# Kernel tuning notes

Hardware: AMD Instinct MI355X
Metric: run time of the kernel (lower is better)

Reference implementation:

```python
import jax, jax.numpy as jnp
import numpy as np

B, J, D, T = 4096, 22, 3, 50  # batch, joints, xyz dims, seq_len
N = J * D                     # 66 channels
LW = 3                        # local_window
TAU = 5.0
EPS = 1e-5


def _chain_adj_mask(n):
    m = np.zeros((n, n), dtype=np.float32)
    for i in range(n - 1):
        m[i, i + 1] = 1.0
        m[i + 1, i] = 1.0
    return m


def _band_mask(t, w):
    i = np.arange(t)
    return (np.abs(i[:, None] - i[None, :]) <= w).astype(np.float32)


def setup_inputs() -> dict:
    key = jax.random.key(0)
    ks = jax.random.split(key, 9)
    x = jax.random.normal(ks[0], (B, N, T), dtype=jnp.float32)
    adj = jnp.eye(J, dtype=jnp.float32) + 0.1 * jax.random.normal(ks[1], (J, J), dtype=jnp.float32)
    adj_t = 0.1 * jax.random.normal(ks[2], (T, T), dtype=jnp.float32)
    adj_jc = 0.1 * jax.random.normal(ks[3], (J, D, D), dtype=jnp.float32)
    adj_tj = 0.1 * jax.random.normal(ks[4], (N, T, T), dtype=jnp.float32)
    mlp = jax.random.normal(ks[5], (T, 4), dtype=jnp.float32)
    w_update = 1e-2 * jax.random.normal(ks[6], (T, T), dtype=jnp.float32)
    b_update = jnp.zeros((T,), dtype=jnp.float32)
    alpha = jnp.ones((1, N, 1), dtype=jnp.float32)
    beta = jnp.zeros((1, N, 1), dtype=jnp.float32)
    adj_mask = jnp.asarray(_chain_adj_mask(J))
    traj_mask = jnp.asarray(_band_mask(T, LW))
    u = jax.random.uniform(ks[7], (B, 4), minval=1e-6, maxval=1.0 - 1e-6, dtype=jnp.float32)
    gumbels = -jnp.log(-jnp.log(u))
    return {"x": x, "adj": adj, "adj_t": adj_t, "adj_jc": adj_jc, "adj_tj": adj_tj,
            "mlp": mlp, "w_update": w_update, "b_update": b_update,
            "alpha": alpha, "beta": beta, "adj_mask": adj_mask,
            "traj_mask": traj_mask, "gumbels": gumbels}


def reference(x, adj, adj_t, adj_jc, adj_tj, mlp, w_update, b_update,
              alpha, beta, adj_mask, traj_mask, gumbels):
    xr = x.reshape(B, J, D, T)
    # spatial GC: masked joint-joint adjacency
    x1 = jnp.einsum('vj,bjct->bvct', adj * adj_mask, xr).reshape(B, N, T)
    # temporal GC: banded time-time adjacency shared over channels
    x2 = jnp.einsum('ft,bnt->bnf', adj_t * traj_mask, x)
    # joint-channel GC: per-joint 3x3 channel mixing
    x3 = jnp.einsum('jkc,bjct->bjkt', adj_jc, xr).reshape(B, N, T)
    # spatio-temporal GC: per-channel banded time-time adjacency
    x4 = jnp.einsum('nft,bnt->bnf', adj_tj * traj_mask[None], x)
    # gate: mean-pool over channels -> [B,T] @ [T,4], hard gumbel-softmax
    prob = x.mean(axis=1) @ mlp
    y = jax.nn.softmax((prob + gumbels) / TAU, axis=-1)
    y_hard = jax.nn.one_hot(jnp.argmax(y, axis=-1), 4, dtype=y.dtype)
    gate = y_hard + y - jax.lax.stop_gradient(y)  # straight-through
    # option 0 is zeros, so only options 1..3 contribute
    x_ = (gate[:, 1, None, None] * x2
          + gate[:, 2, None, None] * x3
          + gate[:, 3, None, None] * x4)
    # update linear along time axis
    x_ = (x1 + x_) @ w_update.T + b_update
    # spatial LayerNorm over channel axis
    mean = x_.mean(axis=1, keepdims=True)
    var = ((x_ - mean) ** 2).mean(axis=1, keepdims=True)
    x_ = (x_ - mean) / jnp.sqrt(var + EPS) * alpha + beta
    return x + x_
```

## Files before the change

kernel.cpp:

```cpp
#include <hip/hip_runtime.h>


typedef __attribute__((ext_vector_type(8))) short short8_t;
typedef __attribute__((ext_vector_type(4))) float f32x4_t;

__device__ __forceinline__ unsigned short f2bf(float f) {
    unsigned u = __float_as_uint(f);
    u += 0x7fffu + ((u >> 16) & 1u);
    return (unsigned short)(u >> 16);
}
__device__ __forceinline__ float bf2f(unsigned us) {
    return __uint_as_float(us << 16);
}

#define XLD(nn, tt) (*(const uint2*)((const char*)xbf + (((((nn) << 6) + (tt)) << 1) ^ (((nn) & 7) << 4))))

__global__ __launch_bounds__(256) void pack_kernel(
    const float* __restrict__ adj_t,
    const float* __restrict__ adj_tj,
    unsigned short* __restrict__ ws)
{
    int i = blockIdx.x * 256 + threadIdx.x;
    if (i < 400) {
        int f = i >> 3, j = i & 7;
        int tt = f - 3 + j;
        float v = (j < 7 && tt >= 0 && tt < 50) ? adj_t[f * 50 + tt] : 0.f;
        ws[i] = f2bf(v);
    } else if (i < 26800) {
        int e = i - 400;
        int nf = e >> 3, j = e & 7;
        int f = nf % 50;
        int tt = f - 3 + j;
        float v = (j < 7 && tt >= 0 && tt < 50) ? adj_tj[(size_t)nf * 50 + tt] : 0.f;
        ws[i] = f2bf(v);
    }
}

__global__ __launch_bounds__(256, 2) void dyn_kernel(
    const float* __restrict__ x,
    const float* __restrict__ adj,
    const float* __restrict__ adj_t,
    const float* __restrict__ adj_jc,
    const float* __restrict__ adj_tj,
    const float* __restrict__ mlp,
    const float* __restrict__ w_update,
    const float* __restrict__ alpha,
    const float* __restrict__ beta,
    const float* __restrict__ gumbels,
    const unsigned short* __restrict__ wpack,
    int packed,
    float* __restrict__ out)
{
    __shared__ unsigned short xbf[66 * 64];
    __shared__ unsigned short zbf[66 * 64];
    __shared__ float wsum[16];
    __shared__ float as[66], bs[66];

    const int b    = blockIdx.x;
    const int tid  = threadIdx.x;
    const int lane = tid & 63;
    const int wv   = tid >> 6;
    const int li   = lane & 15;
    const int lq   = lane >> 4;
    const int f    = wv * 16 + li;
    const float* __restrict__ xb = x + (size_t)b * 3300;

    const float4 gv = *(const float4*)(gumbels + (size_t)b * 4);

    int sn[4], st0[4], sv[4];
    float cwm[4], cwp[4];
    #pragma unroll
    for (int r = 0; r < 4; ++r) {
        int i = tid + (r << 8);
        if (r == 3 && i > 857) i = 857;
        int n = i / 13, q = i - n * 13;
        sn[r] = n; st0[r] = q * 4;
        int v = n / 3; sv[r] = v;
        cwm[r] = (v > 0)  ? adj[v * 22 + v - 1] : 0.f;
        cwp[r] = (v < 21) ? adj[v * 22 + v + 1] : 0.f;
    }

    short8_t bfrag0, bfrag1;
    #pragma unroll
    for (int j = 0; j < 8; ++j) {
        int k0 = 8 * lq + j;
        int k1 = 32 + 8 * lq + j;
        float v0 = (f < 50) ? w_update[f * 50 + k0] : 0.f;
        float v1 = (f < 50 && k1 < 50) ? w_update[f * 50 + k1] : 0.f;
        bfrag0[j] = (short)f2bf(v0);
        bfrag1[j] = (short)f2bf(v1);
    }

    for (int i = tid; i < 198; i += 256) {
        int n = i / 3, p = i - n * 3;
        int t0 = 52 + p * 4;
        int byteoff = ((n * 64 + t0) * 2) ^ ((n & 7) << 4);
        uint2 z2; z2.x = 0u; z2.y = 0u;
        *(uint2*)((char*)xbf + byteoff) = z2;
        *(uint2*)((char*)zbf + byteoff) = z2;
    }
    if (tid < 66) { as[tid] = alpha[tid]; bs[tid] = beta[tid]; }

    float2 xa[4], xc[4];
    #pragma unroll
    for (int r = 0; r < 4; ++r) {
        int off = sn[r] * 50 + st0[r];
        xa[r] = *(const float2*)(xb + off);
        int off2 = off + 2; if (off2 > 3298) off2 = 3298;
        xc[r] = *(const float2*)(xb + off2);
    }
    float4 pl = {0.f, 0.f, 0.f, 0.f};
    const float4* __restrict__ mlp4 = (const float4*)mlp;
    #pragma unroll
    for (int r = 0; r < 4; ++r) {
        int n = sn[r], t0 = st0[r];
        bool full = (t0 < 48);
        float v0 = xa[r].x, v1 = xa[r].y;
        float v2 = full ? xc[r].x : 0.f;
        float v3 = full ? xc[r].y : 0.f;
        float4 m0 = mlp4[t0], m1 = mlp4[t0 + 1];
        int i2 = t0 + 2; if (i2 > 49) i2 = 49;
        int i3 = t0 + 3; if (i3 > 49) i3 = 49;
        float4 m2 = mlp4[i2], m3 = mlp4[i3];
        if (r < 3 || tid < 90) {
            pl.x += v0 * m0.x + v1 * m1.x + v2 * m2.x + v3 * m3.x;
            pl.y += v0 * m0.y + v1 * m1.y + v2 * m2.y + v3 * m3.y;
            pl.z += v0 * m0.z + v1 * m1.z + v2 * m2.z + v3 * m3.z;
            pl.w += v0 * m0.w + v1 * m1.w + v2 * m2.w + v3 * m3.w;
        }
        uint2 pk;
        pk.x = (unsigned)f2bf(v0) | ((unsigned)f2bf(v1) << 16);
        pk.y = (unsigned)f2bf(v2) | ((unsigned)f2bf(v3) << 16);
        *(uint2*)((char*)xbf + (((n * 64 + t0) * 2) ^ ((n & 7) << 4))) = pk;
    }
    #pragma unroll
    for (int d = 1; d < 64; d <<= 1) {
        pl.x += __shfl_xor(pl.x, d, 64);
        pl.y += __shfl_xor(pl.y, d, 64);
        pl.z += __shfl_xor(pl.z, d, 64);
        pl.w += __shfl_xor(pl.w, d, 64);
    }
    if (lane == 0) *(float4*)&wsum[wv * 4] = pl;
    __syncthreads();

    int g;
    {
        float4 s0 = *(const float4*)&wsum[0],  s1 = *(const float4*)&wsum[4];
        float4 s2 = *(const float4*)&wsum[8],  s3 = *(const float4*)&wsum[12];
        const float inv = 1.0f / 66.0f;
        float l0 = (s0.x + s1.x + s2.x + s3.x) * inv + gv.x;
        float l1 = (s0.y + s1.y + s2.y + s3.y) * inv + gv.y;
        float l2 = (s0.z + s1.z + s2.z + s3.z) * inv + gv.z;
        float l3 = (s0.w + s1.w + s2.w + s3.w) * inv + gv.w;
        g = 0; float bv = l0;
        if (l1 > bv) { bv = l1; g = 1; }
        if (l2 > bv) { bv = l2; g = 2; }
        if (l3 > bv) { bv = l3; g = 3; }
    }

    if (g == 1 || g == 3) {
        uint4 w0[4], w1[4];
        auto loadrows = [&](int r, uint4* dst) {
            if (packed) {
                const uint4* wt4 = (const uint4*)
                    ((g == 1) ? wpack : wpack + 400 + (size_t)sn[r] * 400);
                #pragma unroll
                for (int k = 0; k < 4; ++k) {
                    int ff = st0[r] + k; if (ff > 49) ff = 49;
                    dst[k] = wt4[ff];
                }
            } else {
                const float* rb = (g == 1) ? adj_t : (adj_tj + (size_t)sn[r] * 2500);
                #pragma unroll
                for (int k = 0; k < 4; ++k) {
                    int ff = st0[r] + k; if (ff > 49) ff = 49;
                    float w[8];
                    #pragma unroll
                    for (int j = 0; j < 8; ++j) {
                        int tt = ff - 3 + j;
                        w[j] = (j < 7 && tt >= 0 && tt < 50) ? rb[ff * 50 + tt] : 0.f;
                    }
                    uint4 u;
                    u.x = (unsigned)f2bf(w[0]) | ((unsigned)f2bf(w[1]) << 16);
                    u.y = (unsigned)f2bf(w[2]) | ((unsigned)f2bf(w[3]) << 16);
                    u.z = (unsigned)f2bf(w[4]) | ((unsigned)f2bf(w[5]) << 16);
                    u.w = (unsigned)f2bf(w[6]) | ((unsigned)f2bf(w[7]) << 16);
                    dst[k] = u;
                }
            }
        };
        loadrows(0, w0);
        #pragma unroll
        for (int r = 0; r < 4; ++r) {
            uint4* wcur = (r & 1) ? w1 : w0;
            uint4* wnxt = (r & 1) ? w0 : w1;
            if (r < 3) loadrows(r + 1, wnxt);
            int n = sn[r], t0 = st0[r];
            uint2 pm = {0u, 0u}, pp = {0u, 0u};
            if (n >= 3)  pm = XLD(n - 3, t0);
            if (n <= 62) pp = XLD(n + 3, t0);
            float acc0 = cwm[r] * bf2f(pm.x & 0xffff) + cwp[r] * bf2f(pp.x & 0xffff);
            float acc1 = cwm[r] * bf2f(pm.x >> 16)    + cwp[r] * bf2f(pp.x >> 16);
            float acc2 = cwm[r] * bf2f(pm.y & 0xffff) + cwp[r] * bf2f(pp.y & 0xffff);
            float acc3 = cwm[r] * bf2f(pm.y >> 16)    + cwp[r] * bf2f(pp.y >> 16);
            float xr[12];
            if (t0 >= 4) {
                uint2 p0 = XLD(n, t0 - 4);
                xr[0] = bf2f(p0.x & 0xffff); xr[1] = bf2f(p0.x >> 16);
                xr[2] = bf2f(p0.y & 0xffff); xr[3] = bf2f(p0.y >> 16);
            } else { xr[0] = 0.f; xr[1] = 0.f; xr[2] = 0.f; xr[3] = 0.f; }
            {
                uint2 p1 = XLD(n, t0);
                xr[4] = bf2f(p1.x & 0xffff); xr[5] = bf2f(p1.x >> 16);
                xr[6] = bf2f(p1.y & 0xffff); xr[7] = bf2f(p1.y >> 16);
            }
            {
                uint2 p2 = XLD(n, t0 + 4);
                xr[8]  = bf2f(p2.x & 0xffff); xr[9]  = bf2f(p2.x >> 16);
                xr[10] = bf2f(p2.y & 0xffff); xr[11] = bf2f(p2.y >> 16);
            }
            #pragma unroll
            for (int j = 0; j < 4; ++j) {
                int ff = t0 + j;
                if (ff < 50) {
                    uint4 u = wcur[j];
                    float a = bf2f(u.x & 0xffff) * xr[j + 1]
                            + bf2f(u.x >> 16)    * xr[j + 2]
                            + bf2f(u.y & 0xffff) * xr[j + 3]
                            + bf2f(u.y >> 16)    * xr[j + 4]
                            + bf2f(u.z & 0xffff) * xr[j + 5]
                            + bf2f(u.z >> 16)    * xr[j + 6]
                            + bf2f(u.w & 0xffff) * xr[j + 7];
                    if (j == 0) acc0 += a; else if (j == 1) acc1 += a;
                    else if (j == 2) acc2 += a; else acc3 += a;
                }
            }
            uint2 pk;
            pk.x = (unsigned)f2bf(acc0) | ((unsigned)f2bf(acc1) << 16);
            pk.y = (unsigned)f2bf(acc2) | ((unsigned)f2bf(acc3) << 16);
            *(uint2*)((char*)zbf + (((n * 64 + t0) * 2) ^ ((n & 7) << 4))) = pk;
        }
    } else {
        #pragma unroll
        for (int r = 0; r < 4; ++r) {
            int n = sn[r], t0 = st0[r], v = sv[r];
            uint2 pm = {0u, 0u}, pp = {0u, 0u};
            if (n >= 3)  pm = XLD(n - 3, t0);
            if (n <= 62) pp = XLD(n + 3, t0);
            float acc0 = cwm[r] * bf2f(pm.x & 0xffff) + cwp[r] * bf2f(pp.x & 0xffff);
            float acc1 = cwm[r] * bf2f(pm.x >> 16)    + cwp[r] * bf2f(pp.x >> 16);
            float acc2 = cwm[r] * bf2f(pm.y & 0xffff) + cwp[r] * bf2f(pp.y & 0xffff);
            float acc3 = cwm[r] * bf2f(pm.y >> 16)    + cwp[r] * bf2f(pp.y >> 16);
            if (g == 2) {
                int c = n - v * 3;
                const float* ajc = adj_jc + (size_t)(v * 3 + c) * 3;
                #pragma unroll
                for (int cc = 0; cc < 3; ++cc) {
                    float w = ajc[cc];
                    uint2 p = XLD(v * 3 + cc, t0);
                    acc0 += w * bf2f(p.x & 0xffff); acc1 += w * bf2f(p.x >> 16);
                    acc2 += w * bf2f(p.y & 0xffff); acc3 += w * bf2f(p.y >> 16);
                }
            }
            uint2 pk;
            pk.x = (unsigned)f2bf(acc0) | ((unsigned)f2bf(acc1) << 16);
            pk.y = (unsigned)f2bf(acc2) | ((unsigned)f2bf(acc3) << 16);
            *(uint2*)((char*)zbf + (((n * 64 + t0) * 2) ^ ((n & 7) << 4))) = pk;
        }
    }
    __syncthreads();

    f32x4_t dacc[5];
    #pragma unroll
    for (int mt = 0; mt < 5; ++mt) dacc[mt] = (f32x4_t){0.f, 0.f, 0.f, 0.f};

    #pragma unroll
    for (int ks = 0; ks < 2; ++ks) {
        short8_t bfrag = ks ? bfrag1 : bfrag0;
        #pragma unroll
        for (int mt = 0; mt < 5; ++mt) {
            int m = mt * 16 + li;
            short8_t afrag = {0, 0, 0, 0, 0, 0, 0, 0};
            if (m < 66)
                afrag = *(const short8_t*)((const char*)zbf + (((m * 64 + 8 * lq + 32 * ks) * 2) ^ ((m & 7) << 4)));
            dacc[mt] = __builtin_amdgcn_mfma_f32_16x16x32_bf16(afrag, bfrag, dacc[mt], 0, 0, 0);
        }
    }

    float S = 0.f, SS = 0.f;
    #pragma unroll
    for (int mt = 0; mt < 5; ++mt) {
        #pragma unroll
        for (int r = 0; r < 4; ++r) {
            int m = mt * 16 + lq * 4 + r;
            if (mt < 4 || m < 66) { float d = dacc[mt][r]; S += d; SS += d * d; }
        }
    }
    S  += __shfl_xor(S, 16, 64);  S  += __shfl_xor(S, 32, 64);
    SS += __shfl_xor(SS, 16, 64); SS += __shfl_xor(SS, 32, 64);
    const float mean = S * (1.f / 66.f);
    const float var  = SS * (1.f / 66.f) - mean * mean;
    const float rstd = rsqrtf(var + 1e-5f);

    if (f < 50) {
        float* __restrict__ ob = out + (size_t)b * 3300;
        #pragma unroll
        for (int mt = 0; mt < 5; ++mt) {
            #pragma unroll
            for (int r = 0; r < 4; ++r) {
                int m = mt * 16 + lq * 4 + r;
                if (mt < 4 || m < 66) {
                    unsigned short xu = *(const unsigned short*)
                        ((const char*)xbf + (((m * 64 + f) * 2) ^ ((m & 7) << 4)));
                    float xv = bf2f((unsigned)xu);
                    float xn = (dacc[mt][r] - mean) * rstd;
                    ob[m * 50 + f] = xv + xn * as[m] + bs[m];
                }
            }
        }
    }
}

extern "C" void kernel_launch(void* const* d_in, const int* in_sizes, int n_in,
                              void* d_out, int out_size, void* d_ws, size_t ws_size,
                              hipStream_t stream) {
    (void)in_sizes; (void)n_in; (void)out_size;
    const float* x        = (const float*)d_in[0];
    const float* adj      = (const float*)d_in[1];
    const float* adj_t    = (const float*)d_in[2];
    const float* adj_jc   = (const float*)d_in[3];
    const float* adj_tj   = (const float*)d_in[4];
    const float* mlp      = (const float*)d_in[5];
    const float* w_update = (const float*)d_in[6];
    const float* alpha    = (const float*)d_in[8];
    const float* beta     = (const float*)d_in[9];
    const float* gumbels  = (const float*)d_in[12];

    const size_t pack_bytes = (size_t)26800 * sizeof(unsigned short);
    int packed = (d_ws != nullptr && ws_size >= pack_bytes) ? 1 : 0;
    unsigned short* ws = (unsigned short*)d_ws;
    if (packed)
        pack_kernel<<<105, 256, 0, stream>>>(adj_t, adj_tj, ws);

    dyn_kernel<<<4096, 256, 0, stream>>>(x, adj, adj_t, adj_jc, adj_tj, mlp,
                                         w_update, alpha, beta, gumbels,
                                         ws, packed, (float*)d_out);
}
```

Measured before the change: 58.56 us.

## Process two batch samples per block to amortize setup and weight loads

Each block now handles two consecutive batch elements, with double-sized LDS buffers for the bf16 input and intermediate tiles. The per-block setup (index tables, w_update B-fragments, alpha/beta, LDS padding) is shared across both samples, and both samples' global loads are issued up front to raise memory-level parallelism. The grid is halved to 2048 blocks, which doubles LDS use per block and raises register pressure. That can lower occupancy and leave the tail less evenly spread across CUs.

New measurement: 66.04 us. 1.13x slower.

```diff
diff --git a/kernel.cpp b/kernel.cpp
--- a/kernel.cpp
+++ b/kernel.cpp
@@ -12,8 +12,9 @@
 __device__ __forceinline__ float bf2f(unsigned us) {
     return __uint_as_float(us << 16);
 }
-
-#define XLD(nn, tt) (*(const uint2*)((const char*)xbf + (((((nn) << 6) + (tt)) << 1) ^ (((nn) & 7) << 4))))
+__device__ __forceinline__ uint2 xld(const unsigned short* base, int n, int t) {
+    return *(const uint2*)((const char*)base + (((n * 64 + t) * 2) ^ ((n & 7) << 4)));
+}
 
 __global__ __launch_bounds__(256) void pack_kernel(
     const float* __restrict__ adj_t,
@@ -51,21 +52,23 @@
     int packed,
     float* __restrict__ out)
 {
-    __shared__ unsigned short xbf[66 * 64];
-    __shared__ unsigned short zbf[66 * 64];
-    __shared__ float wsum[16];
+    __shared__ unsigned short xls[2][66 * 64];
+    __shared__ unsigned short zls[2][66 * 64];
+    __shared__ float wsum[2][16];
     __shared__ float as[66], bs[66];
 
-    const int b    = blockIdx.x;
     const int tid  = threadIdx.x;
     const int lane = tid & 63;
     const int wv   = tid >> 6;
     const int li   = lane & 15;
     const int lq   = lane >> 4;
     const int f    = wv * 16 + li;
-    const float* __restrict__ xb = x + (size_t)b * 3300;
-
-    const float4 gv = *(const float4*)(gumbels + (size_t)b * 4);
+    const int b0   = blockIdx.x * 2;
+    const float* __restrict__ xb0 = x + (size_t)b0 * 3300;
+    const float* __restrict__ xb1 = xb0 + 3300;
+
+    const float4 gv0 = *(const float4*)(gumbels + (size_t)b0 * 4);
+    const float4 gv1 = *(const float4*)(gumbels + (size_t)b0 * 4 + 4);
 
     int sn[4], st0[4], sv[4];
     float cwm[4], cwp[4];
@@ -96,225 +99,246 @@
         int t0 = 52 + p * 4;
         int byteoff = ((n * 64 + t0) * 2) ^ ((n & 7) << 4);
         uint2 z2; z2.x = 0u; z2.y = 0u;
-        *(uint2*)((char*)xbf + byteoff) = z2;
-        *(uint2*)((char*)zbf + byteoff) = z2;
+        *(uint2*)((char*)xls[0] + byteoff) = z2;
+        *(uint2*)((char*)xls[1] + byteoff) = z2;
+        *(uint2*)((char*)zls[0] + byteoff) = z2;
+        *(uint2*)((char*)zls[1] + byteoff) = z2;
     }
     if (tid < 66) { as[tid] = alpha[tid]; bs[tid] = beta[tid]; }
 
-    float2 xa[4], xc[4];
+    float2 xa[2][4], xc[2][4];
     #pragma unroll
     for (int r = 0; r < 4; ++r) {
         int off = sn[r] * 50 + st0[r];
-        xa[r] = *(const float2*)(xb + off);
         int off2 = off + 2; if (off2 > 3298) off2 = 3298;
-        xc[r] = *(const float2*)(xb + off2);
-    }
-    float4 pl = {0.f, 0.f, 0.f, 0.f};
+        xa[0][r] = *(const float2*)(xb0 + off);
+        xc[0][r] = *(const float2*)(xb0 + off2);
+        xa[1][r] = *(const float2*)(xb1 + off);
+        xc[1][r] = *(const float2*)(xb1 + off2);
+    }
     const float4* __restrict__ mlp4 = (const float4*)mlp;
     #pragma unroll
-    for (int r = 0; r < 4; ++r) {
-        int n = sn[r], t0 = st0[r];
-        bool full = (t0 < 48);
-        float v0 = xa[r].x, v1 = xa[r].y;
-        float v2 = full ? xc[r].x : 0.f;
-        float v3 = full ? xc[r].y : 0.f;
-        float4 m0 = mlp4[t0], m1 = mlp4[t0 + 1];
-        int i2 = t0 + 2; if (i2 > 49) i2 = 49;
-        int i3 = t0 + 3; if (i3 > 49) i3 = 49;
-        float4 m2 = mlp4[i2], m3 = mlp4[i3];
-        if (r < 3 || tid < 90) {
-            pl.x += v0 * m0.x + v1 * m1.x + v2 * m2.x + v3 * m3.x;
-            pl.y += v0 * m0.y + v1 * m1.y + v2 * m2.y + v3 * m3.y;
-            pl.z += v0 * m0.z + v1 * m1.z + v2 * m2.z + v3 * m3.z;
-            pl.w += v0 * m0.w + v1 * m1.w + v2 * m2.w + v3 * m3.w;
-        }
-        uint2 pk;
-        pk.x = (unsigned)f2bf(v0) | ((unsigned)f2bf(v1) << 16);
-        pk.y = (unsigned)f2bf(v2) | ((unsigned)f2bf(v3) << 16);
-        *(uint2*)((char*)xbf + (((n * 64 + t0) * 2) ^ ((n & 7) << 4))) = pk;
-    }
-    #pragma unroll
-    for (int d = 1; d < 64; d <<= 1) {
-        pl.x += __shfl_xor(pl.x, d, 64);
-        pl.y += __shfl_xor(pl.y, d, 64);
-        pl.z += __shfl_xor(pl.z, d, 64);
-        pl.w += __shfl_xor(pl.w, d, 64);
-    }
-    if (lane == 0) *(float4*)&wsum[wv * 4] = pl;
+    for (int bi = 0; bi < 2; ++bi) {
+        float4 pl = {0.f, 0.f, 0.f, 0.f};
+        unsigned short* xbf = xls[bi];
+        #pragma unroll
+        for (int r = 0; r < 4; ++r) {
+            int n = sn[r], t0 = st0[r];
+            bool full = (t0 < 48);
+            float v0 = xa[bi][r].x, v1 = xa[bi][r].y;
+            float v2 = full ? xc[bi][r].x : 0.f;
+            float v3 = full ? xc[bi][r].y : 0.f;
+            float4 m0 = mlp4[t0], m1 = mlp4[t0 + 1];
+            int i2 = t0 + 2; if (i2 > 49) i2 = 49;
+            int i3 = t0 + 3; if (i3 > 49) i3 = 49;
+            float4 m2 = mlp4[i2], m3 = mlp4[i3];
+            if (r < 3 || tid < 90) {
+                pl.x += v0 * m0.x + v1 * m1.x + v2 * m2.x + v3 * m3.x;
+                pl.y += v0 * m0.y + v1 * m1.y + v2 * m2.y + v3 * m3.y;
+                pl.z += v0 * m0.z + v1 * m1.z + v2 * m2.z + v3 * m3.z;
+                pl.w += v0 * m0.w + v1 * m1.w + v2 * m2.w + v3 * m3.w;
+            }
+            uint2 pk;
+            pk.x = (unsigned)f2bf(v0) | ((unsigned)f2bf(v1) << 16);
+            pk.y = (unsigned)f2bf(v2) | ((unsigned)f2bf(v3) << 16);
+            *(uint2*)((char*)xbf + (((n * 64 + t0) * 2) ^ ((n & 7) << 4))) = pk;
+        }
+        #pragma unroll
+        for (int d = 1; d < 64; d <<= 1) {
+            pl.x += __shfl_xor(pl.x, d, 64);
+            pl.y += __shfl_xor(pl.y, d, 64);
+            pl.z += __shfl_xor(pl.z, d, 64);
+            pl.w += __shfl_xor(pl.w, d, 64);
+        }
+        if (lane == 0) *(float4*)&wsum[bi][wv * 4] = pl;
+    }
     __syncthreads();
 
-    int g;
-    {
-        float4 s0 = *(const float4*)&wsum[0],  s1 = *(const float4*)&wsum[4];
-        float4 s2 = *(const float4*)&wsum[8],  s3 = *(const float4*)&wsum[12];
+    int gg[2];
+    #pragma unroll
+    for (int bi = 0; bi < 2; ++bi) {
+        float4 s0 = *(const float4*)&wsum[bi][0],  s1 = *(const float4*)&wsum[bi][4];
+        float4 s2 = *(const float4*)&wsum[bi][8],  s3 = *(const float4*)&wsum[bi][12];
+        float4 gvv = bi ? gv1 : gv0;
         const float inv = 1.0f / 66.0f;
-        float l0 = (s0.x + s1.x + s2.x + s3.x) * inv + gv.x;
-        float l1 = (s0.y + s1.y + s2.y + s3.y) * inv + gv.y;
-        float l2 = (s0.z + s1.z + s2.z + s3.z) * inv + gv.z;
-        float l3 = (s0.w + s1.w + s2.w + s3.w) * inv + gv.w;
-        g = 0; float bv = l0;
+        float l0 = (s0.x + s1.x + s2.x + s3.x) * inv + gvv.x;
+        float l1 = (s0.y + s1.y + s2.y + s3.y) * inv + gvv.y;
+        float l2 = (s0.z + s1.z + s2.z + s3.z) * inv + gvv.z;
+        float l3 = (s0.w + s1.w + s2.w + s3.w) * inv + gvv.w;
+        int g = 0; float bv = l0;
         if (l1 > bv) { bv = l1; g = 1; }
         if (l2 > bv) { bv = l2; g = 2; }
         if (l3 > bv) { bv = l3; g = 3; }
-    }
-
-    if (g == 1 || g == 3) {
-        uint4 w0[4], w1[4];
-        auto loadrows = [&](int r, uint4* dst) {
-            if (packed) {
-                const uint4* wt4 = (const uint4*)
-                    ((g == 1) ? wpack : wpack + 400 + (size_t)sn[r] * 400);
+        gg[bi] = g;
+    }
+
+    #pragma unroll
+    for (int bi = 0; bi < 2; ++bi) {
+        const int g = gg[bi];
+        const unsigned short* xbf = xls[bi];
+        unsigned short* zbf = zls[bi];
+        if (g == 1 || g == 3) {
+            uint4 w0[4], w1[4];
+            auto loadrows = [&](int r, uint4* dst) {
+                if (packed) {
+                    const uint4* wt4 = (const uint4*)
+                        ((g == 1) ? wpack : wpack + 400 + (size_t)sn[r] * 400);
+                    #pragma unroll
+                    for (int k = 0; k < 4; ++k) {
+                        int ff = st0[r] + k; if (ff > 49) ff = 49;
+                        dst[k] = wt4[ff];
+                    }
+                } else {
+                    const float* rb = (g == 1) ? adj_t : (adj_tj + (size_t)sn[r] * 2500);
+                    #pragma unroll
+                    for (int k = 0; k < 4; ++k) {
+                        int ff = st0[r] + k; if (ff > 49) ff = 49;
+                        float w[8];
+                        #pragma unroll
+                        for (int j = 0; j < 8; ++j) {
+                            int tt = ff - 3 + j;
+                            w[j] = (j < 7 && tt >= 0 && tt < 50) ? rb[ff * 50 + tt] : 0.f;
+                        }
+                        uint4 u;
+                        u.x = (unsigned)f2bf(w[0]) | ((unsigned)f2bf(w[1]) << 16);
+                        u.y = (unsigned)f2bf(w[2]) | ((unsigned)f2bf(w[3]) << 16);
+                        u.z = (unsigned)f2bf(w[4]) | ((unsigned)f2bf(w[5]) << 16);
+                        u.w = (unsigned)f2bf(w[6]) | ((unsigned)f2bf(w[7]) << 16);
+                        dst[k] = u;
+                    }
+                }
+            };
+            loadrows(0, w0);
+            #pragma unroll
+            for (int r = 0; r < 4; ++r) {
+                uint4* wcur = (r & 1) ? w1 : w0;
+                uint4* wnxt = (r & 1) ? w0 : w1;
+                if (r < 3) loadrows(r + 1, wnxt);
+                int n = sn[r], t0 = st0[r];
+                uint2 pm = {0u, 0u}, pp = {0u, 0u};
+                if (n >= 3)  pm = xld(xbf, n - 3, t0);
+                if (n <= 62) pp = xld(xbf, n + 3, t0);
+                float acc0 = cwm[r] * bf2f(pm.x & 0xffff) + cwp[r] * bf2f(pp.x & 0xffff);
+                float acc1 = cwm[r] * bf2f(pm.x >> 16)    + cwp[r] * bf2f(pp.x >> 16);
+                float acc2 = cwm[r] * bf2f(pm.y & 0xffff) + cwp[r] * bf2f(pp.y & 0xffff);
+                float acc3 = cwm[r] * bf2f(pm.y >> 16)    + cwp[r] * bf2f(pp.y >> 16);
+                float xr[12];
+                if (t0 >= 4) {
+                    uint2 p0 = xld(xbf, n, t0 - 4);
+                    xr[0] = bf2f(p0.x & 0xffff); xr[1] = bf2f(p0.x >> 16);
+                    xr[2] = bf2f(p0.y & 0xffff); xr[3] = bf2f(p0.y >> 16);
+                } else { xr[0] = 0.f; xr[1] = 0.f; xr[2] = 0.f; xr[3] = 0.f; }
+                {
+                    uint2 p1 = xld(xbf, n, t0);
+                    xr[4] = bf2f(p1.x & 0xffff); xr[5] = bf2f(p1.x >> 16);
+                    xr[6] = bf2f(p1.y & 0xffff); xr[7] = bf2f(p1.y >> 16);
+                }
+                {
+                    uint2 p2 = xld(xbf, n, t0 + 4);
+                    xr[8]  = bf2f(p2.x & 0xffff); xr[9]  = bf2f(p2.x >> 16);
+                    xr[10] = bf2f(p2.y & 0xffff); xr[11] = bf2f(p2.y >> 16);
+                }
                 #pragma unroll
-                for (int k = 0; k < 4; ++k) {
-                    int ff = st0[r] + k; if (ff > 49) ff = 49;
-                    dst[k] = wt4[ff];
-                }
-            } else {
-                const float* rb = (g == 1) ? adj_t : (adj_tj + (size_t)sn[r] * 2500);
-                #pragma unroll
-                for (int k = 0; k < 4; ++k) {
-                    int ff = st0[r] + k; if (ff > 49) ff = 49;
-                    float w[8];
+                for (int j = 0; j < 4; ++j) {
+                    int ff = t0 + j;
+                    if (ff < 50) {
+                        uint4 u = wcur[j];
+                        float a = bf2f(u.x & 0xffff) * xr[j + 1]
+                                + bf2f(u.x >> 16)    * xr[j + 2]
+                                + bf2f(u.y & 0xffff) * xr[j + 3]
+                                + bf2f(u.y >> 16)    * xr[j + 4]
+                                + bf2f(u.z & 0xffff) * xr[j + 5]
+                                + bf2f(u.z >> 16)    * xr[j + 6]
+                                + bf2f(u.w & 0xffff) * xr[j + 7];
+                        if (j == 0) acc0 += a; else if (j == 1) acc1 += a;
+                        else if (j == 2) acc2 += a; else acc3 += a;
+                    }
+                }
+                uint2 pk;
+                pk.x = (unsigned)f2bf(acc0) | ((unsigned)f2bf(acc1) << 16);
+                pk.y = (unsigned)f2bf(acc2) | ((unsigned)f2bf(acc3) << 16);
+                *(uint2*)((char*)zbf + (((n * 64 + t0) * 2) ^ ((n & 7) << 4))) = pk;
+            }
+        } else {
+            #pragma unroll
+            for (int r = 0; r < 4; ++r) {
+                int n = sn[r], t0 = st0[r], v = sv[r];
+                uint2 pm = {0u, 0u}, pp = {0u, 0u};
+                if (n >= 3)  pm = xld(xbf, n - 3, t0);
+                if (n <= 62) pp = xld(xbf, n + 3, t0);
+                float acc0 = cwm[r] * bf2f(pm.x & 0xffff) + cwp[r] * bf2f(pp.x & 0xffff);
+                float acc1 = cwm[r] * bf2f(pm.x >> 16)    + cwp[r] * bf2f(pp.x >> 16);
+                float acc2 = cwm[r] * bf2f(pm.y & 0xffff) + cwp[r] * bf2f(pp.y & 0xffff);
+                float acc3 = cwm[r] * bf2f(pm.y >> 16)    + cwp[r] * bf2f(pp.y >> 16);
+                if (g == 2) {
+                    int c = n - v * 3;
+                    const float* ajc = adj_jc + (size_t)(v * 3 + c) * 3;
                     #pragma unroll
-                    for (int j = 0; j < 8; ++j) {
-                        int tt = ff - 3 + j;
-                        w[j] = (j < 7 && tt >= 0 && tt < 50) ? rb[ff * 50 + tt] : 0.f;
-                    }
-                    uint4 u;
-                    u.x = (unsigned)f2bf(w[0]) | ((unsigned)f2bf(w[1]) << 16);
-                    u.y = (unsigned)f2bf(w[2]) | ((unsigned)f2bf(w[3]) << 16);
-                    u.z = (unsigned)f2bf(w[4]) | ((unsigned)f2bf(w[5]) << 16);
-                    u.w = (unsigned)f2bf(w[6]) | ((unsigned)f2bf(w[7]) << 16);
-                    dst[k] = u;
-                }
-            }
-        };
-        loadrows(0, w0);
-        #pragma unroll
-        for (int r = 0; r < 4; ++r) {
-            uint4* wcur = (r & 1) ? w1 : w0;
-            uint4* wnxt = (r & 1) ? w0 : w1;
-            if (r < 3) loadrows(r + 1, wnxt);
-            int n = sn[r], t0 = st0[r];
-            uint2 pm = {0u, 0u}, pp = {0u, 0u};
-            if (n >= 3)  pm = XLD(n - 3, t0);
-            if (n <= 62) pp = XLD(n + 3, t0);
-            float acc0 = cwm[r] * bf2f(pm.x & 0xffff) + cwp[r] * bf2f(pp.x & 0xffff);
-            float acc1 = cwm[r] * bf2f(pm.x >> 16)    + cwp[r] * bf2f(pp.x >> 16);
-            float acc2 = cwm[r] * bf2f(pm.y & 0xffff) + cwp[r] * bf2f(pp.y & 0xffff);
-            float acc3 = cwm[r] * bf2f(pm.y >> 16)    + cwp[r] * bf2f(pp.y >> 16);
-            float xr[12];
-            if (t0 >= 4) {
-                uint2 p0 = XLD(n, t0 - 4);
-                xr[0] = bf2f(p0.x & 0xffff); xr[1] = bf2f(p0.x >> 16);
-                xr[2] = bf2f(p0.y & 0xffff); xr[3] = bf2f(p0.y >> 16);
-            } else { xr[0] = 0.f; xr[1] = 0.f; xr[2] = 0.f; xr[3] = 0.f; }
-            {
-                uint2 p1 = XLD(n, t0);
-                xr[4] = bf2f(p1.x & 0xffff); xr[5] = bf2f(p1.x >> 16);
-                xr[6] = bf2f(p1.y & 0xffff); xr[7] = bf2f(p1.y >> 16);
-            }
-            {
-                uint2 p2 = XLD(n, t0 + 4);
-                xr[8]  = bf2f(p2.x & 0xffff); xr[9]  = bf2f(p2.x >> 16);
-                xr[10] = bf2f(p2.y & 0xffff); xr[11] = bf2f(p2.y >> 16);
-            }
-            #pragma unroll
-            for (int j = 0; j < 4; ++j) {
-                int ff = t0 + j;
-                if (ff < 50) {
-                    uint4 u = wcur[j];
-                    float a = bf2f(u.x & 0xffff) * xr[j + 1]
-                            + bf2f(u.x >> 16)    * xr[j + 2]
-                            + bf2f(u.y & 0xffff) * xr[j + 3]
-                            + bf2f(u.y >> 16)    * xr[j + 4]
-                            + bf2f(u.z & 0xffff) * xr[j + 5]
-                            + bf2f(u.z >> 16)    * xr[j + 6]
-                            + bf2f(u.w & 0xffff) * xr[j + 7];
-                    if (j == 0) acc0 += a; else if (j == 1) acc1 += a;
-                    else if (j == 2) acc2 += a; else acc3 += a;
-                }
-            }
-            uint2 pk;
-            pk.x = (unsigned)f2bf(acc0) | ((unsigned)f2bf(acc1) << 16);
-            pk.y = (unsigned)f2bf(acc2) | ((unsigned)f2bf(acc3) << 16);
-            *(uint2*)((char*)zbf + (((n * 64 + t0) * 2) ^ ((n & 7) << 4))) = pk;
-        }
-    } else {
-        #pragma unroll
-        for (int r = 0; r < 4; ++r) {
-            int n = sn[r], t0 = st0[r], v = sv[r];
-            uint2 pm = {0u, 0u}, pp = {0u, 0u};
-            if (n >= 3)  pm = XLD(n - 3, t0);
-            if (n <= 62) pp = XLD(n + 3, t0);
-            float acc0 = cwm[r] * bf2f(pm.x & 0xffff) + cwp[r] * bf2f(pp.x & 0xffff);
-            float acc1 = cwm[r] * bf2f(pm.x >> 16)    + cwp[r] * bf2f(pp.x >> 16);
-            float acc2 = cwm[r] * bf2f(pm.y & 0xffff) + cwp[r] * bf2f(pp.y & 0xffff);
-            float acc3 = cwm[r] * bf2f(pm.y >> 16)    + cwp[r] * bf2f(pp.y >> 16);
-            if (g == 2) {
-                int c = n - v * 3;
-                const float* ajc = adj_jc + (size_t)(v * 3 + c) * 3;
-                #pragma unroll
-                for (int cc = 0; cc < 3; ++cc) {
-                    float w = ajc[cc];
-                    uint2 p = XLD(v * 3 + cc, t0);
-                    acc0 += w * bf2f(p.x & 0xffff); acc1 += w * bf2f(p.x >> 16);
-                    acc2 += w * bf2f(p.y & 0xffff); acc3 += w * bf2f(p.y >> 16);
-                }
-            }
-            uint2 pk;
-            pk.x = (unsigned)f2bf(acc0) | ((unsigned)f2bf(acc1) << 16);
-            pk.y = (unsigned)f2bf(acc2) | ((unsigned)f2bf(acc3) << 16);
-            *(uint2*)((char*)zbf + (((n * 64 + t0) * 2) ^ ((n & 7) << 4))) = pk;
+                    for (int cc = 0; cc < 3; ++cc) {
+                        float w = ajc[cc];
+                        uint2 p = xld(xbf, v * 3 + cc, t0);
+                        acc0 += w * bf2f(p.x & 0xffff); acc1 += w * bf2f(p.x >> 16);
+                        acc2 += w * bf2f(p.y & 0xffff); acc3 += w * bf2f(p.y >> 16);
+                    }
+                }
+                uint2 pk;
+                pk.x = (unsigned)f2bf(acc0) | ((unsigned)f2bf(acc1) << 16);
+                pk.y = (unsigned)f2bf(acc2) | ((unsigned)f2bf(acc3) << 16);
+                *(uint2*)((char*)zbf + (((n * 64 + t0) * 2) ^ ((n & 7) << 4))) = pk;
+            }
         }
     }
     __syncthreads();
 
-    f32x4_t dacc[5];
-    #pragma unroll
-    for (int mt = 0; mt < 5; ++mt) dacc[mt] = (f32x4_t){0.f, 0.f, 0.f, 0.f};
-
-    #pragma unroll
-    for (int ks = 0; ks < 2; ++ks) {
-        short8_t bfrag = ks ? bfrag1 : bfrag0;
-        #pragma unroll
-        for (int mt = 0; mt < 5; ++mt) {
-            int m = mt * 16 + li;
-            short8_t afrag = {0, 0, 0, 0, 0, 0, 0, 0};
-            if (m < 66)
-                afrag = *(const short8_t*)((const char*)zbf + (((m * 64 + 8 * lq + 32 * ks) * 2) ^ ((m & 7) << 4)));
-            dacc[mt] = __builtin_amdgcn_mfma_f32_16x16x32_bf16(afrag, bfrag, dacc[mt], 0, 0, 0);
-        }
-    }
-
-    float S = 0.f, SS = 0.f;
-    #pragma unroll
-    for (int mt = 0; mt < 5; ++mt) {
-        #pragma unroll
-        for (int r = 0; r < 4; ++r) {
-            int m = mt * 16 + lq * 4 + r;
-            if (mt < 4 || m < 66) { float d = dacc[mt][r]; S += d; SS += d * d; }
-        }
-    }
-    S  += __shfl_xor(S, 16, 64);  S  += __shfl_xor(S, 32, 64);
-    SS += __shfl_xor(SS, 16, 64); SS += __shfl_xor(SS, 32, 64);
-    const float mean = S * (1.f / 66.f);
-    const float var  = SS * (1.f / 66.f) - mean * mean;
-    const float rstd = rsqrtf(var + 1e-5f);
-
-    if (f < 50) {
-        float* __restrict__ ob = out + (size_t)b * 3300;
+    #pragma unroll
+    for (int bi = 0; bi < 2; ++bi) {
+        const unsigned short* xbf = xls[bi];
+        const unsigned short* zbf = zls[bi];
+        f32x4_t dacc[5];
+        #pragma unroll
+        for (int mt = 0; mt < 5; ++mt) dacc[mt] = (f32x4_t){0.f, 0.f, 0.f, 0.f};
+        #pragma unroll
+        for (int ks = 0; ks < 2; ++ks) {
+            short8_t bfrag = ks ? bfrag1 : bfrag0;
+            #pragma unroll
+            for (int mt = 0; mt < 5; ++mt) {
+                int m = mt * 16 + li;
+                short8_t afrag = {0, 0, 0, 0, 0, 0, 0, 0};
+                if (m < 66)
+                    afrag = *(const short8_t*)((const char*)zbf + (((m * 64 + 8 * lq + 32 * ks) * 2) ^ ((m & 7) << 4)));
+                dacc[mt] = __builtin_amdgcn_mfma_f32_16x16x32_bf16(afrag, bfrag, dacc[mt], 0, 0, 0);
+            }
+        }
+
+        float S = 0.f, SS = 0.f;
         #pragma unroll
         for (int mt = 0; mt < 5; ++mt) {
             #pragma unroll
             for (int r = 0; r < 4; ++r) {
                 int m = mt * 16 + lq * 4 + r;
-                if (mt < 4 || m < 66) {
-                    unsigned short xu = *(const unsigned short*)
-                        ((const char*)xbf + (((m * 64 + f) * 2) ^ ((m & 7) << 4)));
-                    float xv = bf2f((unsigned)xu);
-                    float xn = (dacc[mt][r] - mean) * rstd;
-                    ob[m * 50 + f] = xv + xn * as[m] + bs[m];
+                if (mt < 4 || m < 66) { float d = dacc[mt][r]; S += d; SS += d * d; }
+            }
+        }
+        S  += __shfl_xor(S, 16, 64);  S  += __shfl_xor(S, 32, 64);
+        SS += __shfl_xor(SS, 16, 64); SS += __shfl_xor(SS, 32, 64);
+        const float mean = S * (1.f / 66.f);
+        const float var  = SS * (1.f / 66.f) - mean * mean;
+        const float rstd = rsqrtf(var + 1e-5f);
+
+        if (f < 50) {
+            float* __restrict__ ob = out + (size_t)(b0 + bi) * 3300;
+            #pragma unroll
+            for (int mt = 0; mt < 5; ++mt) {
+                #pragma unroll
+                for (int r = 0; r < 4; ++r) {
+                    int m = mt * 16 + lq * 4 + r;
+                    if (mt < 4 || m < 66) {
+                        unsigned short xu = *(const unsigned short*)
+                            ((const char*)xbf + (((m * 64 + f) * 2) ^ ((m & 7) << 4)));
+                        float xv = bf2f((unsigned)xu);
+                        float xn = (dacc[mt][r] - mean) * rstd;
+                        ob[m * 50 + f] = xv + xn * as[m] + bs[m];
+                    }
                 }
             }
         }
@@ -342,7 +366,7 @@
     if (packed)
         pack_kernel<<<105, 256, 0, stream>>>(adj_t, adj_tj, ws);
 
-    dyn_kernel<<<4096, 256, 0, stream>>>(x, adj, adj_t, adj_jc, adj_tj, mlp,
+    dyn_kernel<<<2048, 256, 0, stream>>>(x, adj, adj_t, adj_jc, adj_tj, mlp,
                                          w_update, alpha, beta, gumbels,
                                          ws, packed, (float*)d_out);
 }
```
